# Kernel optimization log

Hardware: AMD Instinct MI355X
Metric: run time of the kernel (lower is better)

## Reference

```python
import jax, jax.numpy as jnp
import numpy as np

N_NODES = 100000
N_EDGES = 1600000
D_FEAT = 256
UNITS = 128
N_SUP = 2


def setup_inputs() -> dict:
    key = jax.random.key(0)
    ks = jax.random.split(key, 8)
    x = jax.random.normal(ks[0], (N_NODES, D_FEAT), dtype=jnp.float32)
    edge_vals = jax.random.uniform(ks[1], (N_SUP, N_EDGES), dtype=jnp.float32)
    W = jax.random.normal(ks[2], (N_SUP, D_FEAT, UNITS), dtype=jnp.float32) * 0.06  # ~glorot scale
    b = jnp.zeros((N_SUP, UNITS), dtype=jnp.float32)
    W_gate = jax.random.normal(ks[3], (N_SUP, D_FEAT, 1), dtype=jnp.float32) * 0.1
    b_gate = jnp.zeros((N_SUP, 1), dtype=jnp.float32)
    edge_rows = jax.random.randint(ks[4], (N_SUP, N_EDGES), 0, N_NODES, dtype=jnp.int32)
    edge_cols = jax.random.randint(ks[5], (N_SUP, N_EDGES), 0, N_NODES, dtype=jnp.int32)
    return {"x": x, "edge_vals": edge_vals, "W": W, "b": b,
            "W_gate": W_gate, "b_gate": b_gate,
            "edge_rows": edge_rows, "edge_cols": edge_cols}


def _spmm(rows, cols, vals, dense):
    # A @ dense where A is COO sparse [N, N]; dense is [N, U]
    msgs = vals[:, None] * dense[cols]  # [E, U]
    return jax.ops.segment_sum(msgs, rows, num_segments=N_NODES)


def reference(x, edge_vals, W, b, W_gate, b_gate, edge_rows, edge_cols):
    out = jnp.zeros((N_NODES, UNITS), dtype=x.dtype)
    for i in range(N_SUP):  # small fixed number of structurally distinct supports
        pre_sup = x @ W[i] + b[i]                           # [N, UNITS]
        g = jax.nn.sigmoid(x @ W_gate[i] + b_gate[i])       # [N, 1]
        out = out + _spmm(edge_rows[i], edge_cols[i], edge_vals[i], g * pre_sup)
    return jax.nn.relu(out)
```

## Files before the change

kernel.cpp:

```cpp
#include <hip/hip_runtime.h>
#include <hip/hip_bf16.h>

#define N_NODES 100000
#define N_EDGES 1600000
#define D_FEAT  256
#define UNITS   128
#define SLAB    48
#define NBKT    98
#define BKT_CAP 18432
#define NTILES  (N_NODES / 16)
#define NPAIR   ((NTILES + 7) / 8)
#define GEMM_BLKS (98 * 16)
#define SPLIT_BLKS 391
#define B_SHORTS (8 * 9 * 64 * 8)

typedef __attribute__((ext_vector_type(8))) short bf16x8;
typedef __attribute__((ext_vector_type(4))) float f32x4;
typedef __attribute__((ext_vector_type(2))) float f32x2;

__global__ __launch_bounds__(256) void pack_w_kernel(
    const float* __restrict__ W, const float* __restrict__ Wg,
    __hip_bfloat16* __restrict__ Bp) {
  const int idx = blockIdx.x * 256 + threadIdx.x;
  if (idx >= 2 * 8 * 9 * 64 * 8) return;
  const int j    = idx & 7;
  const int lane = (idx >> 3) & 63;
  const int cf   = (idx >> 9) % 9;
  const int ks   = (idx >> 9) / 9 % 8;
  const int s    = idx / (8 * 9 * 64 * 8);
  const int k    = ks * 32 + (lane >> 4) * 8 + j;
  float v;
  if (cf < 8) {
    const int col = cf * 16 + (lane & 15);
    v = W[((size_t)s * D_FEAT + k) * UNITS + col];
  } else {
    v = ((lane & 15) == 0) ? Wg[(size_t)s * D_FEAT + k] : 0.f;
  }
  Bp[idx] = __float2bfloat16(v);
}

__device__ __forceinline__ void gemm_body(
    const float* __restrict__ x, const __hip_bfloat16* __restrict__ Bp,
    const float* __restrict__ b, const float* __restrict__ bg,
    __hip_bfloat16* __restrict__ h, short* __restrict__ Blds, int pairBase) {
  const int tid  = threadIdx.x;
  const int lane = tid & 63;
  const int wave = tid >> 6;
  const int l15  = lane & 15;
  const int l4   = lane >> 4;
  const int tb   = pairBase * 8 + wave;
  const int rowbase = tb * 16;

  const int r0 = min(rowbase + l15, N_NODES - 1);
  const float4* __restrict__ a0p =
      (const float4*)(x + (size_t)r0 * D_FEAT) + l4 * 2;

  float4 xa[16];
#pragma unroll
  for (int ks = 0; ks < 8; ++ks) {
    xa[2 * ks]     = a0p[ks * 8];
    xa[2 * ks + 1] = a0p[ks * 8 + 1];
  }

  const float4* __restrict__ bp4 = (const float4*)Bp;
  float4*       __restrict__ ld4 = (float4*)Blds;
#pragma unroll
  for (int i = 0; i < 9; ++i)
    ld4[i * 512 + tid] = bp4[i * 512 + tid];
  __syncthreads();

  f32x4 acc[9];
#pragma unroll
  for (int cf = 0; cf < 9; ++cf) acc[cf] = (f32x4){0.f, 0.f, 0.f, 0.f};

#pragma unroll
  for (int ks = 0; ks < 8; ++ks) {
    const float4 lo = xa[2 * ks], hi = xa[2 * ks + 1];
    union { bf16x8 v; __hip_bfloat16 e[8]; } fa;
    fa.e[0] = __float2bfloat16(lo.x); fa.e[1] = __float2bfloat16(lo.y);
    fa.e[2] = __float2bfloat16(lo.z); fa.e[3] = __float2bfloat16(lo.w);
    fa.e[4] = __float2bfloat16(hi.x); fa.e[5] = __float2bfloat16(hi.y);
    fa.e[6] = __float2bfloat16(hi.z); fa.e[7] = __float2bfloat16(hi.w);
#pragma unroll
    for (int cf = 0; cf < 9; ++cf) {
      const bf16x8 fb = *(const bf16x8*)(Blds + ((ks * 9 + cf) * 64 + lane) * 8);
      acc[cf] = __builtin_amdgcn_mfma_f32_16x16x32_bf16(fa.v, fb, acc[cf], 0, 0, 0);
    }
  }

  const float bgv = bg[0];
  float bv[8];
#pragma unroll
  for (int cf = 0; cf < 8; ++cf) bv[cf] = b[cf * 16 + l15];

#pragma unroll
  for (int r = 0; r < 4; ++r) {
    const float gp = __shfl(acc[8][r], lane & 48);
    const float g  = 1.f / (1.f + __expf(-(gp + bgv)));
    const int row  = rowbase + l4 * 4 + r;
    if (row < N_NODES) {
#pragma unroll
      for (int cf = 0; cf < 8; ++cf) {
        const float val = g * (acc[cf][r] + bv[cf]);
        h[(size_t)row * UNITS + cf * 16 + l15] = __float2bfloat16(val);
      }
    }
  }
}

__device__ __forceinline__ void split_body(
    const int* __restrict__ rows, const int* __restrict__ cols,
    const float* __restrict__ vals, int* __restrict__ cursor,
    int2* __restrict__ grouped, int* __restrict__ shm, int chunk) {
  int* hist = shm;
  int* base = shm + NBKT;
  const int t  = threadIdx.x;
  const int e0 = chunk * 4096;

  for (int i = t; i < NBKT; i += 512) hist[i] = 0;
  __syncthreads();

  int rloc[8];
#pragma unroll
  for (int i = 0; i < 8; ++i) {
    const int e = e0 + i * 512 + t;
    if (e < N_EDGES) {
      rloc[i] = __builtin_nontemporal_load(rows + e);
      atomicAdd(&hist[rloc[i] >> 10], 1);
    }
  }
  __syncthreads();

  for (int i = t; i < NBKT; i += 512) {
    const int c = hist[i];
    base[i] = c ? atomicAdd(&cursor[i], c) : 0;
    hist[i] = 0;
  }
  __syncthreads();

#pragma unroll
  for (int i = 0; i < 8; ++i) {
    const int e = e0 + i * 512 + t;
    if (e < N_EDGES) {
      const int r   = rloc[i];
      const int bkt = r >> 10;
      const int pos = base[bkt] + atomicAdd(&hist[bkt], 1);
      if (pos < BKT_CAP) {
        const int   c = __builtin_nontemporal_load(cols + e);
        const float v = __builtin_nontemporal_load(vals + e);
        grouped[(size_t)bkt * BKT_CAP + pos] =
            make_int2((r & 1023) | (c << 10), __float2int_rn(v * 32767.f));
      }
    }
  }
}

__global__ __launch_bounds__(512, 4) void mega_kernel(
    const float* __restrict__ x, const __hip_bfloat16* __restrict__ Bp,
    const float* __restrict__ b, const float* __restrict__ bg,
    __hip_bfloat16* __restrict__ h0, __hip_bfloat16* __restrict__ h1,
    const int* __restrict__ er, const int* __restrict__ ec,
    const float* __restrict__ ev,
    int* __restrict__ cursor0, int* __restrict__ cursor1,
    int2* __restrict__ grouped0, int2* __restrict__ grouped1) {
  __shared__ short Blds[B_SHORTS];
  const int j = blockIdx.x;
  if (j < GEMM_BLKS) {
    const int r = j & 15;
    const int s = r >> 3;
    const int pairBase = (j >> 4) * 8 + (r & 7);
    if (pairBase >= NPAIR) return;
    gemm_body(x, Bp + (size_t)s * B_SHORTS, b + s * UNITS, bg + s,
              s ? h1 : h0, Blds, pairBase);
  } else {
    const int idx   = j - GEMM_BLKS;
    const int s     = idx >= SPLIT_BLKS;
    const int chunk = s ? idx - SPLIT_BLKS : idx;
    split_body(er + (size_t)s * N_EDGES, ec + (size_t)s * N_EDGES,
               ev + (size_t)s * N_EDGES,
               s ? cursor1 : cursor0, s ? grouped1 : grouped0,
               (int*)Blds, chunk);
  }
}

__global__ __launch_bounds__(512, 4) void gemm_mfma_kernel(
    const float* __restrict__ x, const __hip_bfloat16* __restrict__ Bp,
    const float* __restrict__ b, const float* __restrict__ bg,
    __hip_bfloat16* __restrict__ h) {
  __shared__ short Blds[B_SHORTS];
  gemm_body(x, Bp, b, bg, h, Blds, blockIdx.x);
}

__global__ __launch_bounds__(512) void split512_kernel(
    const int* __restrict__ rows, const int* __restrict__ cols,
    const float* __restrict__ vals, int* __restrict__ cursor,
    int2* __restrict__ grouped) {
  __shared__ int shm[2 * NBKT];
  split_body(rows, cols, vals, cursor, grouped, shm, blockIdx.x);
}

__device__ __forceinline__ void bin_body(
    const int* __restrict__ cursor, const int2* __restrict__ grouped,
    int* __restrict__ deg, unsigned int* __restrict__ slab,
    int* __restrict__ ldeg, int bkt) {
  const int t   = threadIdx.x;
  const int cnt = min(cursor[bkt], BKT_CAP);
  const int rowbase = bkt << 10;

  ldeg[t] = 0;
  __syncthreads();

  const int2* __restrict__ g = grouped + (size_t)bkt * BKT_CAP;
  for (int i = t; i < cnt; i += 1024) {
    const unsigned long long raw =
        __builtin_nontemporal_load((const unsigned long long*)(g + i));
    const int gx = (int)(raw & 0xffffffffu);
    const int gy = (int)(raw >> 32);
    const int rl  = gx & 1023;
    const int pos = atomicAdd(&ldeg[rl], 1);
    if (pos < SLAB)
      slab[(size_t)(rowbase + rl) * SLAB + pos] =
          (((unsigned int)gx >> 10) << 15) | (unsigned int)gy;
  }
  __syncthreads();

  const int row = rowbase + t;
  if (row < N_NODES) {
    const int d    = min(ldeg[t], SLAB);
    const int dpad = min((d + 7) & ~7, SLAB);
    for (int p = d; p < dpad; ++p)
      slab[(size_t)row * SLAB + p] = 0u;
    deg[row] = dpad;
  }
}

__global__ __launch_bounds__(1024) void bin_pair_kernel(
    const int* __restrict__ cursor0, const int2* __restrict__ grouped0,
    int* __restrict__ deg0, unsigned int* __restrict__ slab0,
    const int* __restrict__ cursor1, const int2* __restrict__ grouped1,
    int* __restrict__ deg1, unsigned int* __restrict__ slab1) {
  __shared__ int ldeg[1024];
  const int s   = blockIdx.x & 1;
  const int bkt = blockIdx.x >> 1;
  if (s == 0) bin_body(cursor0, grouped0, deg0, slab0, ldeg, bkt);
  else        bin_body(cursor1, grouped1, deg1, slab1, ldeg, bkt);
}

__global__ __launch_bounds__(1024) void bin_kernel(
    const int* __restrict__ cursor, const int2* __restrict__ grouped,
    int* __restrict__ deg, unsigned int* __restrict__ slab) {
  __shared__ int ldeg[1024];
  bin_body(cursor, grouped, deg, slab, ldeg, blockIdx.x);
}

__global__ __launch_bounds__(256) void gather_fused(
    const int* __restrict__ deg0, const unsigned int* __restrict__ slab0,
    const unsigned int* __restrict__ h0,
    const int* __restrict__ deg1, const unsigned int* __restrict__ slab1,
    const unsigned int* __restrict__ h1,
    float* __restrict__ out) {
  const int wave = threadIdx.x >> 6;
  const int lane = threadIdx.x & 63;
  const int row  = blockIdx.x * 4 + wave;
  const int d0   = deg0[row];
  const int d1   = deg1[row];

  int ent0 = 0, ent1 = 0;
  if (lane < d0) ent0 = (int)__builtin_nontemporal_load(slab0 + (size_t)row * SLAB + lane);
  if (lane < d1) ent1 = (int)__builtin_nontemporal_load(slab1 + (size_t)row * SLAB + lane);

  const float SC = 1.f / 32767.f;
  float2 accA = make_float2(0.f, 0.f);
  float2 accB = make_float2(0.f, 0.f);

  const int nb0 = d0 >> 3;
  const int nb1 = d1 >> 3;
  const int nb  = max(nb0, nb1);

  for (int bi = 0; bi < nb; ++bi) {
    const int e = bi * 8;
    unsigned int u0[8], u1[8];
    float v0[8], v1[8];
    const bool go0 = bi < nb0;
    const bool go1 = bi < nb1;
    if (go0) {
#pragma unroll
      for (int i = 0; i < 8; ++i) {
        const unsigned int w = (unsigned int)__shfl(ent0, e + i);
        v0[i] = (float)(w & 0x7fffu) * SC;
        u0[i] = h0[(size_t)(w >> 15) * 64 + lane];
      }
    }
    if (go1) {
#pragma unroll
      for (int i = 0; i < 8; ++i) {
        const unsigned int w = (unsigned int)__shfl(ent1, e + i);
        v1[i] = (float)(w & 0x7fffu) * SC;
        u1[i] = h1[(size_t)(w >> 15) * 64 + lane];
      }
    }
    if (go0) {
#pragma unroll
      for (int i = 0; i < 8; ++i) {
        float2& a = (i & 1) ? accB : accA;
        a.x += v0[i] * __uint_as_float(u0[i] << 16);
        a.y += v0[i] * __uint_as_float(u0[i] & 0xffff0000u);
      }
    }
    if (go1) {
#pragma unroll
      for (int i = 0; i < 8; ++i) {
        float2& a = (i & 1) ? accB : accA;
        a.x += v1[i] * __uint_as_float(u1[i] << 16);
        a.y += v1[i] * __uint_as_float(u1[i] & 0xffff0000u);
      }
    }
  }

  f32x2 o;
  o.x = fmaxf(accA.x + accB.x, 0.f);
  o.y = fmaxf(accA.y + accB.y, 0.f);
  __builtin_nontemporal_store(o, (f32x2*)out + (size_t)row * 64 + lane);
}

template <int LAST>
__global__ __launch_bounds__(256) void gather_one(
    const int* __restrict__ deg, const unsigned int* __restrict__ slab,
    const unsigned int* __restrict__ hbits, float* __restrict__ out) {
  const int wave = threadIdx.x >> 6;
  const int lane = threadIdx.x & 63;
  const int row  = blockIdx.x * 4 + wave;
  const int d    = deg[row];

  int ent = 0;
  if (lane < d) ent = (int)__builtin_nontemporal_load(slab + (size_t)row * SLAB + lane);

  const float SC = 1.f / 32767.f;
  float2 accA = make_float2(0.f, 0.f);
  float2 accB = make_float2(0.f, 0.f);
  const int nb = d >> 3;
  for (int bi = 0; bi < nb; ++bi) {
    const int e = bi * 8;
    unsigned int u[8];
    float v[8];
#pragma unroll
    for (int i = 0; i < 8; ++i) {
      const unsigned int w = (unsigned int)__shfl(ent, e + i);
      v[i] = (float)(w & 0x7fffu) * SC;
      u[i] = hbits[(size_t)(w >> 15) * 64 + lane];
    }
#pragma unroll
    for (int i = 0; i < 8; ++i) {
      float2& a = (i & 1) ? accB : accA;
      a.x += v[i] * __uint_as_float(u[i] << 16);
      a.y += v[i] * __uint_as_float(u[i] & 0xffff0000u);
    }
  }

  float2 acc = make_float2(accA.x + accB.x, accA.y + accB.y);
  float2* __restrict__ o2 = (float2*)out;
  const size_t oi = (size_t)row * 64 + lane;
  if (LAST) {
    const float2 prev = o2[oi];
    acc.x = fmaxf(prev.x + acc.x, 0.f);
    acc.y = fmaxf(prev.y + acc.y, 0.f);
  }
  o2[oi] = acc;
}

extern "C" void kernel_launch(void* const* d_in, const int* in_sizes, int n_in,
                              void* d_out, int out_size, void* d_ws, size_t ws_size,
                              hipStream_t stream) {
  const float* x         = (const float*)d_in[0];
  const float* edge_vals = (const float*)d_in[1];
  const float* W         = (const float*)d_in[2];
  const float* b         = (const float*)d_in[3];
  const float* Wg        = (const float*)d_in[4];
  const float* bg        = (const float*)d_in[5];
  const int*   er        = (const int*)d_in[6];
  const int*   ec        = (const int*)d_in[7];
  float* out = (float*)d_out;
  char* ws = (char*)d_ws;

  const size_t NEED = 105146624;

  if (ws_size >= NEED) {
    __hip_bfloat16* h0       = (__hip_bfloat16*)ws;
    __hip_bfloat16* h1       = (__hip_bfloat16*)(ws + 25600000);
    int*            deg0     = (int*)(ws + 51200000);
    int*            deg1     = (int*)(ws + 51600000);
    int*            cursor0  = (int*)(ws + 52000000);
    int*            cursor1  = (int*)(ws + 52000512);
    unsigned int*   slab0    = (unsigned int*)(ws + 52001024);
    unsigned int*   slab1    = (unsigned int*)(ws + 71201024);
    int2*           grouped0 = (int2*)(ws + 71201024);
    int2*           grouped1 = (int2*)(ws + 90401024);
    __hip_bfloat16* Bp       = (__hip_bfloat16*)(ws + 104851712);

    pack_w_kernel<<<(2 * 8 * 9 * 64 * 8 + 255) / 256, 256, 0, stream>>>(W, Wg, Bp);
    hipMemsetAsync(cursor0, 0, 1024, stream);

    mega_kernel<<<GEMM_BLKS + 2 * SPLIT_BLKS, 512, 0, stream>>>(
        x, Bp, b, bg, h0, h1, er, ec, edge_vals,
        cursor0, cursor1, grouped0, grouped1);

    bin_kernel<<<NBKT, 1024, 0, stream>>>(cursor0, grouped0, deg0, slab0);
    bin_kernel<<<NBKT, 1024, 0, stream>>>(cursor1, grouped1, deg1, slab1);

    gather_fused<<<N_NODES / 4, 256, 0, stream>>>(
        deg0, slab0, (const unsigned int*)h0,
        deg1, slab1, (const unsigned int*)h1, out);
  } else {
    __hip_bfloat16* h       = (__hip_bfloat16*)ws;
    int*            deg     = (int*)(ws + 25600000);
    int*            cursor  = (int*)(ws + 26000000);
    unsigned int*   slab    = (unsigned int*)(ws + 26000512);
    int2*           grouped = (int2*)(ws + 45200512);
    __hip_bfloat16* Bp      = (__hip_bfloat16*)(ws + 59651200);

    pack_w_kernel<<<(2 * 8 * 9 * 64 * 8 + 255) / 256, 256, 0, stream>>>(W, Wg, Bp);

    for (int s = 0; s < 2; ++s) {
      hipMemsetAsync(cursor, 0, 512, stream);
      gemm_mfma_kernel<<<NPAIR, 512, 0, stream>>>(
          x, Bp + (size_t)s * B_SHORTS, b + (size_t)s * UNITS, bg + s, h);
      split512_kernel<<<SPLIT_BLKS, 512, 0, stream>>>(
          er + (size_t)s * N_EDGES, ec + (size_t)s * N_EDGES,
          edge_vals + (size_t)s * N_EDGES, cursor, grouped);
      bin_kernel<<<NBKT, 1024, 0, stream>>>(cursor, grouped, deg, slab);
      if (s == 0) {
        gather_one<0><<<N_NODES / 4, 256, 0, stream>>>(deg, slab, (const unsigned int*)h, out);
      } else {
        gather_one<1><<<N_NODES / 4, 256, 0, stream>>>(deg, slab, (const unsigned int*)h, out);
      }
    }
  }
}
```

Measured before the change: 243.4 us.

## Process two rows per wave in gather and launch paired binning kernel

```diff
diff --git a/kernel.cpp b/kernel.cpp
--- a/kernel.cpp
+++ b/kernel.cpp
@@ -16,7 +16,6 @@
 
 typedef __attribute__((ext_vector_type(8))) short bf16x8;
 typedef __attribute__((ext_vector_type(4))) float f32x4;
-typedef __attribute__((ext_vector_type(2))) float f32x2;
 
 __global__ __launch_bounds__(256) void pack_w_kernel(
     const float* __restrict__ W, const float* __restrict__ Wg,
@@ -255,72 +254,87 @@
 
 __global__ __launch_bounds__(256) void gather_fused(
     const int* __restrict__ deg0, const unsigned int* __restrict__ slab0,
-    const unsigned int* __restrict__ h0,
+    const uint2* __restrict__ h0,
     const int* __restrict__ deg1, const unsigned int* __restrict__ slab1,
-    const unsigned int* __restrict__ h1,
+    const uint2* __restrict__ h1,
     float* __restrict__ out) {
   const int wave = threadIdx.x >> 6;
   const int lane = threadIdx.x & 63;
-  const int row  = blockIdx.x * 4 + wave;
-  const int d0   = deg0[row];
-  const int d1   = deg1[row];
-
-  int ent0 = 0, ent1 = 0;
-  if (lane < d0) ent0 = (int)__builtin_nontemporal_load(slab0 + (size_t)row * SLAB + lane);
-  if (lane < d1) ent1 = (int)__builtin_nontemporal_load(slab1 + (size_t)row * SLAB + lane);
-
-  const float SC = 1.f / 32767.f;
-  float2 accA = make_float2(0.f, 0.f);
-  float2 accB = make_float2(0.f, 0.f);
+  const int sl   = lane & 31;
+  const int half = lane >> 5;
+  const int row  = blockIdx.x * 8 + wave * 2 + half;
+
+  const int d0 = __builtin_nontemporal_load(deg0 + row);
+  const int d1 = __builtin_nontemporal_load(deg1 + row);
+
+  const unsigned int* __restrict__ s0 = slab0 + (size_t)row * SLAB;
+  const unsigned int* __restrict__ s1 = slab1 + (size_t)row * SLAB;
+  int e0a = 0, e0b = 0, e1a = 0, e1b = 0;
+  if (sl < d0)      e0a = (int)__builtin_nontemporal_load(s0 + sl);
+  if (sl + 32 < d0) e0b = (int)__builtin_nontemporal_load(s0 + 32 + sl);
+  if (sl < d1)      e1a = (int)__builtin_nontemporal_load(s1 + sl);
+  if (sl + 32 < d1) e1b = (int)__builtin_nontemporal_load(s1 + 32 + sl);
 
   const int nb0 = d0 >> 3;
   const int nb1 = d1 >> 3;
-  const int nb  = max(nb0, nb1);
-
-  for (int bi = 0; bi < nb; ++bi) {
+  const int nbw = max(max(nb0, __shfl_xor(nb0, 32)),
+                      max(nb1, __shfl_xor(nb1, 32)));
+
+  float a0 = 0.f, a1 = 0.f, a2 = 0.f, a3 = 0.f;
+
+  for (int bi = 0; bi < nbw; ++bi) {
     const int e = bi * 8;
-    unsigned int u0[8], u1[8];
-    float v0[8], v1[8];
     const bool go0 = bi < nb0;
     const bool go1 = bi < nb1;
+    uint2 u0[8], u1[8];
+    float v0[8], v1[8];
     if (go0) {
 #pragma unroll
       for (int i = 0; i < 8; ++i) {
-        const unsigned int w = (unsigned int)__shfl(ent0, e + i);
-        v0[i] = (float)(w & 0x7fffu) * SC;
-        u0[i] = h0[(size_t)(w >> 15) * 64 + lane];
+        const int src = e + i;
+        const unsigned int w = (unsigned int)(
+            (src < 32) ? __shfl(e0a, src, 32) : __shfl(e0b, src - 32, 32));
+        v0[i] = (float)(w & 0x7fffu);
+        u0[i] = h0[(size_t)(w >> 15) * 32 + sl];
       }
     }
     if (go1) {
 #pragma unroll
       for (int i = 0; i < 8; ++i) {
-        const unsigned int w = (unsigned int)__shfl(ent1, e + i);
-        v1[i] = (float)(w & 0x7fffu) * SC;
-        u1[i] = h1[(size_t)(w >> 15) * 64 + lane];
+        const int src = e + i;
+        const unsigned int w = (unsigned int)(
+            (src < 32) ? __shfl(e1a, src, 32) : __shfl(e1b, src - 32, 32));
+        v1[i] = (float)(w & 0x7fffu);
+        u1[i] = h1[(size_t)(w >> 15) * 32 + sl];
       }
     }
     if (go0) {
 #pragma unroll
       for (int i = 0; i < 8; ++i) {
-        float2& a = (i & 1) ? accB : accA;
-        a.x += v0[i] * __uint_as_float(u0[i] << 16);
-        a.y += v0[i] * __uint_as_float(u0[i] & 0xffff0000u);
+        a0 += v0[i] * __uint_as_float(u0[i].x << 16);
+        a1 += v0[i] * __uint_as_float(u0[i].x & 0xffff0000u);
+        a2 += v0[i] * __uint_as_float(u0[i].y << 16);
+        a3 += v0[i] * __uint_as_float(u0[i].y & 0xffff0000u);
       }
     }
     if (go1) {
 #pragma unroll
       for (int i = 0; i < 8; ++i) {
-        float2& a = (i & 1) ? accB : accA;
-        a.x += v1[i] * __uint_as_float(u1[i] << 16);
-        a.y += v1[i] * __uint_as_float(u1[i] & 0xffff0000u);
-      }
-    }
-  }
-
-  f32x2 o;
-  o.x = fmaxf(accA.x + accB.x, 0.f);
-  o.y = fmaxf(accA.y + accB.y, 0.f);
-  __builtin_nontemporal_store(o, (f32x2*)out + (size_t)row * 64 + lane);
+        a0 += v1[i] * __uint_as_float(u1[i].x << 16);
+        a1 += v1[i] * __uint_as_float(u1[i].x & 0xffff0000u);
+        a2 += v1[i] * __uint_as_float(u1[i].y << 16);
+        a3 += v1[i] * __uint_as_float(u1[i].y & 0xffff0000u);
+      }
+    }
+  }
+
+  const float SC = 1.f / 32767.f;
+  f32x4 o;
+  o.x = fmaxf(a0 * SC, 0.f);
+  o.y = fmaxf(a1 * SC, 0.f);
+  o.z = fmaxf(a2 * SC, 0.f);
+  o.w = fmaxf(a3 * SC, 0.f);
+  __builtin_nontemporal_store(o, (f32x4*)out + (size_t)row * 32 + sl);
 }
 
 template <int LAST>
@@ -346,7 +360,7 @@
 #pragma unroll
     for (int i = 0; i < 8; ++i) {
       const unsigned int w = (unsigned int)__shfl(ent, e + i);
-      v[i] = (float)(w & 0x7fffu) * SC;
+      v[i] = (float)(w & 0x7fffu);
       u[i] = hbits[(size_t)(w >> 15) * 64 + lane];
     }
 #pragma unroll
@@ -357,13 +371,15 @@
     }
   }
 
-  float2 acc = make_float2(accA.x + accB.x, accA.y + accB.y);
+  float2 acc = make_float2((accA.x + accB.x) * SC, (accA.y + accB.y) * SC);
   float2* __restrict__ o2 = (float2*)out;
   const size_t oi = (size_t)row * 64 + lane;
   if (LAST) {
     const float2 prev = o2[oi];
     acc.x = fmaxf(prev.x + acc.x, 0.f);
     acc.y = fmaxf(prev.y + acc.y, 0.f);
+  } else {
+    acc.x = fmaxf(acc.x, 0.f) - fmaxf(acc.x, 0.f) + acc.x;
   }
   o2[oi] = acc;
 }
@@ -382,9 +398,35 @@
   float* out = (float*)d_out;
   char* ws = (char*)d_ws;
 
-  const size_t NEED = 105146624;
-
-  if (ws_size >= NEED) {
+  const size_t NEED2 = 119597312;
+  const size_t NEED  = 105146624;
+
+  if (ws_size >= NEED2) {
+    __hip_bfloat16* h0       = (__hip_bfloat16*)ws;
+    __hip_bfloat16* h1       = (__hip_bfloat16*)(ws + 25600000);
+    int*            deg0     = (int*)(ws + 51200000);
+    int*            deg1     = (int*)(ws + 51600000);
+    int*            cursor0  = (int*)(ws + 52000000);
+    int*            cursor1  = (int*)(ws + 52000512);
+    unsigned int*   slab0    = (unsigned int*)(ws + 52001024);
+    unsigned int*   slab1    = (unsigned int*)(ws + 71201024);
+    int2*           grouped0 = (int2*)(ws + 90401024);
+    int2*           grouped1 = (int2*)(ws + 104851712);
+    __hip_bfloat16* Bp       = (__hip_bfloat16*)(ws + 119302400);
+
+    pack_w_kernel<<<(2 * 8 * 9 * 64 * 8 + 255) / 256, 256, 0, stream>>>(W, Wg, Bp);
+    hipMemsetAsync(cursor0, 0, 1024, stream);
+
+    mega_kernel<<<GEMM_BLKS + 2 * SPLIT_BLKS, 512, 0, stream>>>(
+        x, Bp, b, bg, h0, h1, er, ec, edge_vals,
+        cursor0, cursor1, grouped0, grouped1);
+
+    bin_pair_kernel<<<2 * NBKT, 1024, 0, stream>>>(
+        cursor0, grouped0, deg0, slab0, cursor1, grouped1, deg1, slab1);
+
+    gather_fused<<<N_NODES / 8, 256, 0, stream>>>(
+        deg0, slab0, (const uint2*)h0, deg1, slab1, (const uint2*)h1, out);
+  } else if (ws_size >= NEED) {
     __hip_bfloat16* h0       = (__hip_bfloat16*)ws;
     __hip_bfloat16* h1       = (__hip_bfloat16*)(ws + 25600000);
     int*            deg0     = (int*)(ws + 51200000);
@@ -407,9 +449,8 @@
     bin_kernel<<<NBKT, 1024, 0, stream>>>(cursor0, grouped0, deg0, slab0);
     bin_kernel<<<NBKT, 1024, 0, stream>>>(cursor1, grouped1, deg1, slab1);
 
-    gather_fused<<<N_NODES / 4, 256, 0, stream>>>(
-        deg0, slab0, (const unsigned int*)h0,
-        deg1, slab1, (const unsigned int*)h1, out);
+    gather_fused<<<N_NODES / 8, 256, 0, stream>>>(
+        deg0, slab0, (const uint2*)h0, deg1, slab1, (const uint2*)h1, out);
   } else {
     __hip_bfloat16* h       = (__hip_bfloat16*)ws;
     int*            deg     = (int*)(ws + 25600000);
```

New measurement: 230.0 us. -5.5%, faster.
